# Kernel tuning notes

Hardware: AMD Instinct MI355X
Metric: run time of the kernel (lower is better)

Reference implementation:

```python
import jax, jax.numpy as jnp
import numpy as np

N_NODES = 50000
N_EDGES = 800000
IN_DIM = 128
HID_DIM = 128
N_CLASSES = 32
X_STEPS = 2
BN_EPS = 1e-5


def _agg(h, src, dst):
    # PyG 'add' aggregation with self-loops: out[i] = sum_{(j->i) in E} h[j] + h[i]
    return jax.ops.segment_sum(h[src], dst, num_segments=h.shape[0]) + h


def setup_inputs() -> dict:
    key = jax.random.key(0)
    ks = jax.random.split(key, 8)
    x = jax.random.normal(ks[0], (N_NODES, IN_DIM), dtype=jnp.float32)
    edge_index = jax.random.randint(ks[1], (2, N_EDGES), 0, N_NODES, dtype=jnp.int64)
    s1 = 1.0 / np.sqrt(IN_DIM)
    W1 = jax.random.uniform(ks[2], (IN_DIM, HID_DIM), jnp.float32, -s1, s1)
    b1 = jax.random.uniform(ks[3], (HID_DIM,), jnp.float32, -s1, s1)
    gamma = jnp.ones((HID_DIM,), jnp.float32)
    beta = jnp.zeros((HID_DIM,), jnp.float32)
    s2 = 1.0 / np.sqrt(HID_DIM)
    W2 = jax.random.uniform(ks[4], (HID_DIM, N_CLASSES), jnp.float32, -s2, s2)
    b2 = jax.random.uniform(ks[5], (N_CLASSES,), jnp.float32, -s2, s2)
    return {"x": x, "edge_index": edge_index, "W1": W1, "b1": b1,
            "gamma": gamma, "beta": beta, "W2": W2, "b2": b2}


def reference(x, edge_index, W1, b1, gamma, beta, W2, b2):
    src, dst = edge_index[0], edge_index[1]
    # conv1: K-step sum aggregation, then Linear
    h = x
    for _ in range(X_STEPS):
        h = _agg(h, src, dst)
    h = h @ W1 + b1
    # BatchNorm (training mode: batch statistics over nodes)
    mu = jnp.mean(h, axis=0)
    var = jnp.mean(jnp.square(h - mu), axis=0)  # biased variance, as torch BN uses
    h = (h - mu) * jax.lax.rsqrt(var + BN_EPS) * gamma + beta
    h = jax.nn.selu(h)
    # dropout p=0.0 -> identity
    # conv2: 1-step aggregation + Linear
    h = _agg(h, src, dst)
    h = h @ W2 + b2
    return jax.nn.softmax(h, axis=1)
```

## Files before the change

kernel.cpp:

```cpp
#include <hip/hip_runtime.h>

#define NN 50000
#define NE 800000
#define DIM 128
#define NC 32
#define CB 782
#define CCH 13
#define EB 8192
#define NBLK 98
#define BN_EPS 1e-5f
#define SELU_ALPHA 1.6732632423543772f
#define SELU_SCALE 1.0507009873554805f

typedef __attribute__((ext_vector_type(8))) short bf16x8;
typedef __attribute__((ext_vector_type(4))) float f32x4;

#define FMA16(acc, hv, w0, w1, w2, w3)                                   \
    acc.x = fmaf(hv.x, w0.x, acc.x); acc.y = fmaf(hv.x, w0.y, acc.y);    \
    acc.z = fmaf(hv.x, w0.z, acc.z); acc.w = fmaf(hv.x, w0.w, acc.w);    \
    acc.x = fmaf(hv.y, w1.x, acc.x); acc.y = fmaf(hv.y, w1.y, acc.y);    \
    acc.z = fmaf(hv.y, w1.z, acc.z); acc.w = fmaf(hv.y, w1.w, acc.w);    \
    acc.x = fmaf(hv.z, w2.x, acc.x); acc.y = fmaf(hv.z, w2.y, acc.y);    \
    acc.z = fmaf(hv.z, w2.z, acc.z); acc.w = fmaf(hv.z, w2.w, acc.w);    \
    acc.x = fmaf(hv.w, w3.x, acc.x); acc.y = fmaf(hv.w, w3.y, acc.y);    \
    acc.z = fmaf(hv.w, w3.z, acc.z); acc.w = fmaf(hv.w, w3.w, acc.w);

#define BNSELU1(v)                                                        \
    v = v > 0.f ? SELU_SCALE * v : SELU_SCALE * SELU_ALPHA * (__expf(v) - 1.f);
#define BNSELU4(hv, sc, sh)                                               \
    hv.x = fmaf(hv.x, sc.x, sh.x); BNSELU1(hv.x)                          \
    hv.y = fmaf(hv.y, sc.y, sh.y); BNSELU1(hv.y)                          \
    hv.z = fmaf(hv.z, sc.z, sh.z); BNSELU1(hv.z)                          \
    hv.w = fmaf(hv.w, sc.w, sh.w); BNSELU1(hv.w)

__device__ __forceinline__ float bf_lo(unsigned u) { return __uint_as_float(u << 16); }
__device__ __forceinline__ float bf_hi(unsigned u) { return __uint_as_float(u & 0xffff0000u); }
__device__ __forceinline__ unsigned bf_round(float a) {
    unsigned ba = __float_as_uint(a);
    return (ba + 0x7fffu + ((ba >> 16) & 1u)) >> 16;
}
__device__ __forceinline__ unsigned pack_bf16(float a, float b) {
    return bf_round(a) | (bf_round(b) << 16);
}

__device__ __forceinline__ int edge_flag(const int* raw) {
    int v = raw[2 * (threadIdx.x & 63) + 1];
    unsigned long long b = __ballot(v == 0);
    return b == 0xFFFFFFFFFFFFFFFFULL;
}

#define CVT_BLOCKS 6250
#define PREP_BLOCKS (CVT_BLOCKS + 65)
__global__ __launch_bounds__(256) void k_prep(
    const float4* __restrict__ in, uint2* __restrict__ out,
    const float* __restrict__ W1, ushort* __restrict__ w1t,
    float* __restrict__ z, const void* __restrict__ raw, int* __restrict__ cnt) {
    __shared__ int lh[CB];
    int bid = blockIdx.x, tid = threadIdx.x;
    if (bid < CVT_BLOCKS) {
        int i = bid * 256 + tid;
        float4 v = in[i];
        out[i] = make_uint2(pack_bf16(v.x, v.y), pack_bf16(v.z, v.w));
    } else if (bid < CVT_BLOCKS + 64) {
        int i = (bid - CVT_BLOCKS) * 256 + tid;
        int k = i >> 7, n = i & 127;
        w1t[n * 136 + k] = (ushort)bf_round(W1[i]);
    } else if (bid == CVT_BLOCKS + 64) {
        z[tid] = 0.f;
    } else {
        int blk = bid - PREP_BLOCKS;
        for (int t = tid; t < CB; t += 256) lh[t] = 0;
        __syncthreads();
        int f = edge_flag((const int*)raw);
        const long long* r64 = (const long long*)raw;
        const int* r32 = (const int*)raw;
        int e0 = blk * EB;
        int n = min(EB, NE - e0);
        for (int i = tid; i < n; i += 256) {
            int d = f ? (int)r64[NE + e0 + i] : r32[NE + e0 + i];
            atomicAdd(&lh[d >> 6], 1);
        }
        __syncthreads();
        for (int t = tid; t < CB; t += 256) cnt[t * NBLK + blk] = lh[t];
    }
}

__global__ void k_colscan(int* __restrict__ cnt, int* __restrict__ tot) {
    int b = blockIdx.x;
    int* row = cnt + b * NBLK;
    int l = threadIdx.x;
    int p0 = 2 * l, p1 = 2 * l + 1;
    int a0 = (p0 < NBLK) ? row[p0] : 0;
    int a1 = (p1 < NBLK) ? row[p1] : 0;
    int s = a0 + a1, inc = s;
    #pragma unroll
    for (int off = 1; off < 64; off <<= 1) {
        int u = __shfl_up(inc, off, 64);
        if (l >= off) inc += u;
    }
    int ex = inc - s;
    if (p0 < NBLK) row[p0] = ex;
    if (p1 < NBLK) row[p1] = ex + a0;
    if (l == 63) tot[b] = inc;
}

__global__ void k_cscan(const int* __restrict__ tot, int* __restrict__ cbase,
                        int* __restrict__ rowptr) {
    int lane = threadIdx.x;
    int base = lane * CCH;
    int loc[CCH];
    int s = 0;
    #pragma unroll
    for (int i = 0; i < CCH; ++i) {
        int idx = base + i;
        int v = (idx < CB) ? tot[idx] : 0;
        loc[i] = s; s += v;
    }
    int inc = s;
    #pragma unroll
    for (int off = 1; off < 64; off <<= 1) {
        int u = __shfl_up(inc, off, 64);
        if (lane >= off) inc += u;
    }
    int ex = inc - s;
    #pragma unroll
    for (int i = 0; i < CCH; ++i) {
        int idx = base + i;
        if (idx < CB) cbase[idx] = ex + loc[i];
    }
    if (lane == 63) { cbase[CB] = inc; rowptr[NN] = NE; }
}

__global__ __launch_bounds__(256) void k_cscatter2(const void* __restrict__ raw,
                                                   const int* __restrict__ cnt,
                                                   const int* __restrict__ cbase,
                                                   unsigned* __restrict__ pairs) {
    __shared__ int lh[CB], lbase[CB], lcur[CB], gbase[CB];
    __shared__ unsigned lp[EB];
    int blk = blockIdx.x, tid = threadIdx.x;
    for (int t = tid; t < CB; t += 256) {
        lh[t] = 0;
        gbase[t] = cbase[t] + cnt[t * NBLK + blk];
    }
    __syncthreads();
    int f = edge_flag((const int*)raw);
    const long long* r64 = (const long long*)raw;
    const int* r32 = (const int*)raw;
    int e0 = blk * EB;
    int n = min(EB, NE - e0);
    for (int i = tid; i < n; i += 256) {
        int d = f ? (int)r64[NE + e0 + i] : r32[NE + e0 + i];
        atomicAdd(&lh[d >> 6], 1);
    }
    __syncthreads();
    if (tid < 64) {
        int base = tid * CCH;
        int loc[CCH];
        int s = 0;
        #pragma unroll
        for (int i = 0; i < CCH; ++i) {
            int idx = base + i;
            int v = (idx < CB) ? lh[idx] : 0;
            loc[i] = s; s += v;
        }
        int inc = s;
        #pragma unroll
        for (int off = 1; off < 64; off <<= 1) {
            int u = __shfl_up(inc, off, 64);
            if (tid >= off) inc += u;
        }
        int ex = inc - s;
        #pragma unroll
        for (int i = 0; i < CCH; ++i) {
            int idx = base + i;
            if (idx < CB) lbase[idx] = ex + loc[i];
        }
    }
    __syncthreads();
    for (int t = tid; t < CB; t += 256) lcur[t] = lbase[t];
    __syncthreads();
    for (int i = tid; i < n; i += 256) {
        int d = f ? (int)r64[NE + e0 + i] : r32[NE + e0 + i];
        int sv = f ? (int)r64[e0 + i] : r32[e0 + i];
        int b = d >> 6;
        int p = atomicAdd(&lcur[b], 1);
        lp[p] = (unsigned)sv | ((unsigned)(d & 63) << 16) | ((unsigned)b << 22);
    }
    __syncthreads();
    for (int i = tid; i < n; i += 256) {
        unsigned pr = lp[i];
        int b = pr >> 22;
        pairs[gbase[b] + (i - lbase[b])] = pr;
    }
}

__global__ __launch_bounds__(256) void k_bucket(const unsigned* __restrict__ pairs,
                                                const int* __restrict__ cbase,
                                                int* __restrict__ rowptr,
                                                ushort* __restrict__ eidx) {
    __shared__ int cnt[64], cur[64];
    int b = blockIdx.x;
    int tid = threadIdx.x;
    if (tid < 64) cnt[tid] = 0;
    __syncthreads();
    int lo = cbase[b], hi = cbase[b + 1];
    for (int i = lo + tid; i < hi; i += 256)
        atomicAdd(&cnt[(pairs[i] >> 16) & 63], 1);
    __syncthreads();
    if (tid < 64) {
        int v = cnt[tid];
        int inc = v;
        #pragma unroll
        for (int off = 1; off < 64; off <<= 1) {
            int u = __shfl_up(inc, off, 64);
            if (tid >= off) inc += u;
        }
        int ex = inc - v;
        cur[tid] = ex;
        int node = b * 64 + tid;
        if (node < NN) rowptr[node] = lo + ex;
    }
    __syncthreads();
    for (int i = lo + tid; i < hi; i += 256) {
        unsigned pr = pairs[i];
        int p = atomicAdd(&cur[(pr >> 16) & 63], 1);
        eidx[lo + p] = (ushort)(pr & 0xFFFFu);
    }
}

__global__ __launch_bounds__(256) void k_gather_bf(const unsigned* __restrict__ in,
                                                   unsigned* __restrict__ out,
                                                   const int* __restrict__ rowptr,
                                                   const ushort* __restrict__ eidx) {
    int node = blockIdx.x * 4 + (threadIdx.x >> 6);
    if (node >= NN) return;
    int lane = threadIdx.x & 63;
    unsigned su = in[(size_t)node * 64 + lane];
    float2 acc = {bf_lo(su), bf_hi(su)};
    int b = rowptr[node], e = rowptr[node + 1];
    int j = b;
    for (; j + 7 < e; j += 8) {
        int s0 = eidx[j],     s1 = eidx[j + 1], s2 = eidx[j + 2], s3 = eidx[j + 3];
        int s4 = eidx[j + 4], s5 = eidx[j + 5], s6 = eidx[j + 6], s7 = eidx[j + 7];
        unsigned u0 = in[(size_t)s0 * 64 + lane];
        unsigned u1 = in[(size_t)s1 * 64 + lane];
        unsigned u2 = in[(size_t)s2 * 64 + lane];
        unsigned u3 = in[(size_t)s3 * 64 + lane];
        unsigned u4 = in[(size_t)s4 * 64 + lane];
        unsigned u5 = in[(size_t)s5 * 64 + lane];
        unsigned u6 = in[(size_t)s6 * 64 + lane];
        unsigned u7 = in[(size_t)s7 * 64 + lane];
        acc.x += bf_lo(u0) + bf_lo(u1) + bf_lo(u2) + bf_lo(u3)
               + bf_lo(u4) + bf_lo(u5) + bf_lo(u6) + bf_lo(u7);
        acc.y += bf_hi(u0) + bf_hi(u1) + bf_hi(u2) + bf_hi(u3)
               + bf_hi(u4) + bf_hi(u5) + bf_hi(u6) + bf_hi(u7);
    }
    for (; j + 3 < e; j += 4) {
        int s0 = eidx[j], s1 = eidx[j + 1], s2 = eidx[j + 2], s3 = eidx[j + 3];
        unsigned u0 = in[(size_t)s0 * 64 + lane];
        unsigned u1 = in[(size_t)s1 * 64 + lane];
        unsigned u2 = in[(size_t)s2 * 64 + lane];
        unsigned u3 = in[(size_t)s3 * 64 + lane];
        acc.x += bf_lo(u0) + bf_lo(u1) + bf_lo(u2) + bf_lo(u3);
        acc.y += bf_hi(u0) + bf_hi(u1) + bf_hi(u2) + bf_hi(u3);
    }
    for (; j < e; ++j) {
        unsigned u0 = in[(size_t)eidx[j] * 64 + lane];
        acc.x += bf_lo(u0);
        acc.y += bf_hi(u0);
    }
    out[(size_t)node * 64 + lane] = pack_bf16(acc.x, acc.y);
}

__global__ __launch_bounds__(256) void k_gemm1(
    const unsigned* __restrict__ hBb, const ushort* __restrict__ w1t,
    const float* __restrict__ b1, float* __restrict__ h1,
    float* __restrict__ ssum, float* __restrict__ ssq) {
    __shared__ __align__(16) ushort wT[DIM * 136];
    __shared__ float redS[4 * DIM];
    __shared__ float redQ[4 * DIM];
    int tid = threadIdx.x;
    for (int i = tid; i < DIM * 136 / 8; i += 256)
        ((uint4*)wT)[i] = ((const uint4*)w1t)[i];
    for (int i = tid; i < 4 * DIM; i += 256) { redS[i] = 0.f; redQ[i] = 0.f; }
    __syncthreads();

    int wid = tid >> 6, lane = tid & 63;
    int cl = lane & 15, kg = lane >> 4;
    int tile = blockIdx.x * 4 + wid;
    if (tile < NN / 16) {
        int rbase = tile * 16;
        const uint4* arow = (const uint4*)(hBb + (size_t)(rbase + cl) * 64);
        f32x4 acc[8];
        #pragma unroll
        for (int ct = 0; ct < 8; ++ct) acc[ct] = (f32x4){0.f, 0.f, 0.f, 0.f};
        #pragma unroll
        for (int kk = 0; kk < 4; ++kk) {
            union { uint4 u; bf16x8 f; } a;
            a.u = arow[kk * 4 + kg];
            #pragma unroll
            for (int ct = 0; ct < 8; ++ct) {
                union { uint4 u; bf16x8 f; } bb;
                bb.u = *(const uint4*)&wT[(ct * 16 + cl) * 136 + kk * 32 + kg * 8];
                acc[ct] = __builtin_amdgcn_mfma_f32_16x16x32_bf16(a.f, bb.f, acc[ct], 0, 0, 0);
            }
        }
        #pragma unroll
        for (int ct = 0; ct < 8; ++ct) {
            int col = ct * 16 + cl;
            float bias = b1[col];
            float s = 0.f, q = 0.f;
            #pragma unroll
            for (int i = 0; i < 4; ++i) {
                float v = acc[ct][i] + bias;
                h1[(size_t)(rbase + kg * 4 + i) * DIM + col] = v;
                s += v; q += v * v;
            }
            s += __shfl_xor(s, 16); s += __shfl_xor(s, 32);
            q += __shfl_xor(q, 16); q += __shfl_xor(q, 32);
            if (kg == 0) { redS[wid * DIM + col] = s; redQ[wid * DIM + col] = q; }
        }
    }
    __syncthreads();
    if (tid < DIM) {
        float S = redS[tid] + redS[DIM + tid] + redS[2 * DIM + tid] + redS[3 * DIM + tid];
        float Q = redQ[tid] + redQ[DIM + tid] + redQ[2 * DIM + tid] + redQ[3 * DIM + tid];
        atomicAdd(&ssum[tid], S);
        atomicAdd(&ssq[tid], Q);
    }
}

__global__ __launch_bounds__(256) void k_gemm2(const float* __restrict__ h,
                                               const float* __restrict__ W2,
                                               const float* __restrict__ ssum,
                                               const float* __restrict__ ssq,
                                               const float* __restrict__ gamma,
                                               const float* __restrict__ beta,
                                               unsigned* __restrict__ tb) {
    __shared__ float w[DIM * NC];
    __shared__ float scl[DIM], shl[DIM];
    for (int i = threadIdx.x * 4; i < DIM * NC; i += 1024)
        *(float4*)&w[i] = *(const float4*)&W2[i];
    if (threadIdx.x < DIM) {
        int c = threadIdx.x;
        float mu = ssum[c] / (float)NN;
        float var = ssq[c] / (float)NN - mu * mu;
        float rs = rsqrtf(var + BN_EPS);
        float sc = rs * gamma[c];
        scl[c] = sc;
        shl[c] = beta[c] - mu * sc;
    }
    __syncthreads();

    int c0 = (threadIdx.x & 7) * 4;
    int rg = threadIdx.x >> 3;
    int r0 = blockIdx.x * 128 + rg * 4;
    if (r0 >= NN) return;
    const float* h0 = h + (size_t)r0 * DIM;
    float4 a0 = {0, 0, 0, 0}, a1 = {0, 0, 0, 0}, a2 = {0, 0, 0, 0}, a3 = {0, 0, 0, 0};
    #pragma unroll 4
    for (int k4 = 0; k4 < DIM / 4; ++k4) {
        float4 sc = *(const float4*)&scl[k4 * 4];
        float4 sh = *(const float4*)&shl[k4 * 4];
        float4 hv0 = *(const float4*)&h0[k4 * 4];
        float4 hv1 = *(const float4*)&h0[DIM + k4 * 4];
        float4 hv2 = *(const float4*)&h0[2 * DIM + k4 * 4];
        float4 hv3 = *(const float4*)&h0[3 * DIM + k4 * 4];
        BNSELU4(hv0, sc, sh)
        BNSELU4(hv1, sc, sh)
        BNSELU4(hv2, sc, sh)
        BNSELU4(hv3, sc, sh)
        float4 w0 = *(const float4*)&w[(k4 * 4 + 0) * NC + c0];
        float4 w1 = *(const float4*)&w[(k4 * 4 + 1) * NC + c0];
        float4 w2 = *(const float4*)&w[(k4 * 4 + 2) * NC + c0];
        float4 w3 = *(const float4*)&w[(k4 * 4 + 3) * NC + c0];
        FMA16(a0, hv0, w0, w1, w2, w3)
        FMA16(a1, hv1, w0, w1, w2, w3)
        FMA16(a2, hv2, w0, w1, w2, w3)
        FMA16(a3, hv3, w0, w1, w2, w3)
    }
    ((uint2*)tb)[((size_t)r0 * 16 + c0 / 2) / 2]       = make_uint2(pack_bf16(a0.x, a0.y), pack_bf16(a0.z, a0.w));
    ((uint2*)tb)[((size_t)(r0 + 1) * 16 + c0 / 2) / 2] = make_uint2(pack_bf16(a1.x, a1.y), pack_bf16(a1.z, a1.w));
    ((uint2*)tb)[((size_t)(r0 + 2) * 16 + c0 / 2) / 2] = make_uint2(pack_bf16(a2.x, a2.y), pack_bf16(a2.z, a2.w));
    ((uint2*)tb)[((size_t)(r0 + 3) * 16 + c0 / 2) / 2] = make_uint2(pack_bf16(a3.x, a3.y), pack_bf16(a3.z, a3.w));
}

__global__ __launch_bounds__(256) void k_gsoftmax(const unsigned* __restrict__ tb,
                                                  const float* __restrict__ b2,
                                                  const int* __restrict__ rowptr,
                                                  const ushort* __restrict__ eidx,
                                                  float* __restrict__ out) {
    int node = blockIdx.x * 4 + (threadIdx.x >> 6);
    if (node >= NN) return;
    int lane = threadIdx.x & 63;
    int c2 = lane & 15;
    int g = lane >> 4;
    float2 acc = {0.f, 0.f};
    if (g == 0) {
        unsigned u = tb[(size_t)node * 16 + c2];
        acc.x = bf_lo(u); acc.y = bf_hi(u);
    }
    int b = rowptr[node], e = rowptr[node + 1];
    int j = b + g;
    for (; j + 4 < e; j += 8) {
        int s0 = eidx[j];
        int s1 = eidx[j + 4];
        unsigned u0 = tb[(size_t)s0 * 16 + c2];
        unsigned u1 = tb[(size_t)s1 * 16 + c2];
        acc.x += bf_lo(u0) + bf_lo(u1);
        acc.y += bf_hi(u0) + bf_hi(u1);
    }
    if (j < e) {
        unsigned u = tb[(size_t)eidx[j] * 16 + c2];
        acc.x += bf_lo(u);
        acc.y += bf_hi(u);
    }
    acc.x += __shfl_xor(acc.x, 16); acc.x += __shfl_xor(acc.x, 32);
    acc.y += __shfl_xor(acc.y, 16); acc.y += __shfl_xor(acc.y, 32);
    acc.x += b2[2 * c2];
    acc.y += b2[2 * c2 + 1];
    float m = fmaxf(acc.x, acc.y);
    #pragma unroll
    for (int off = 8; off; off >>= 1) m = fmaxf(m, __shfl_xor(m, off, 16));
    float2 ex = {__expf(acc.x - m), __expf(acc.y - m)};
    float s = ex.x + ex.y;
    #pragma unroll
    for (int off = 8; off; off >>= 1) s += __shfl_xor(s, off, 16);
    float inv = 1.f / s;
    if (g == 0)
        *(float2*)&out[(size_t)node * NC + 2 * c2] = make_float2(ex.x * inv, ex.y * inv);
}

extern "C" void kernel_launch(void* const* d_in, const int* in_sizes, int n_in,
                              void* d_out, int out_size, void* d_ws, size_t ws_size,
                              hipStream_t stream) {
    const float* x     = (const float*)d_in[0];
    const void*  eraw  = d_in[1];
    const float* W1    = (const float*)d_in[2];
    const float* b1    = (const float*)d_in[3];
    const float* gamma = (const float*)d_in[4];
    const float* beta  = (const float*)d_in[5];
    const float* W2    = (const float*)d_in[6];
    const float* b2    = (const float*)d_in[7];
    float* out = (float*)d_out;

    float*    regA = (float*)d_ws;
    unsigned* xb   = (unsigned*)regA;
    unsigned* hAb  = xb + (size_t)NN * 64;
    float*    h1   = regA;
    float*    regB = regA + (size_t)NN * DIM;
    unsigned* pairs= (unsigned*)regB;
    unsigned* hBb  = (unsigned*)regB;
    unsigned* tb   = (unsigned*)(regB + (size_t)NN * 64);
    ushort* eidx = (ushort*)(regB + (size_t)NN * DIM);
    int* rowptr = (int*)(eidx + NE);
    int* cnt    = rowptr + NN + 4;
    int* tot    = cnt + CB * NBLK;
    int* cbase  = tot + 784;
    float* ssum  = (float*)(cbase + 784);
    float* ssq   = ssum + DIM;
    ushort* w1t  = (ushort*)(ssq + DIM);

    k_prep<<<PREP_BLOCKS + NBLK, 256, 0, stream>>>(
        (const float4*)x, (uint2*)xb, W1, w1t, ssum, eraw, cnt);
    k_colscan<<<CB, 64, 0, stream>>>(cnt, tot);
    k_cscan<<<1, 64, 0, stream>>>(tot, cbase, rowptr);
    k_cscatter2<<<NBLK, 256, 0, stream>>>(eraw, cnt, cbase, pairs);
    k_bucket<<<CB, 256, 0, stream>>>(pairs, cbase, rowptr, eidx);

    const int gather_blocks = (NN + 3) / 4;
    k_gather_bf<<<gather_blocks, 256, 0, stream>>>(xb, hAb, rowptr, eidx);
    k_gather_bf<<<gather_blocks, 256, 0, stream>>>(hAb, hBb, rowptr, eidx);
    k_gemm1<<<(NN / 16 + 3) / 4, 256, 0, stream>>>(hBb, w1t, b1, h1, ssum, ssq);
    k_gemm2<<<(NN + 127) / 128, 256, 0, stream>>>(h1, W2, ssum, ssq, gamma, beta, tb);
    k_gsoftmax<<<gather_blocks, 256, 0, stream>>>(tb, b2, rowptr, eidx, out);
}
```

Measured before the change: 202.3 us.

## Merge column and chunk scans via last-block atomic; reuse histogram counts in scatter

Folds the single-block chunk scan into the column-scan kernel: each block bumps a done counter and the last block to finish runs the global scan. This removes one kernel launch. The scan output now goes to a separate cnts array, so the scatter kernel can read the per-block histogram from cnt directly instead of recounting destinations with a second pass and shared atomics. The cost is an extra counter reset, threadfences, and a second count array in the workspace.

```diff
diff --git a/kernel.cpp b/kernel.cpp
--- a/kernel.cpp
+++ b/kernel.cpp
@@ -54,7 +54,8 @@
 __global__ __launch_bounds__(256) void k_prep(
     const float4* __restrict__ in, uint2* __restrict__ out,
     const float* __restrict__ W1, ushort* __restrict__ w1t,
-    float* __restrict__ z, const void* __restrict__ raw, int* __restrict__ cnt) {
+    float* __restrict__ z, int* __restrict__ done,
+    const void* __restrict__ raw, int* __restrict__ cnt) {
     __shared__ int lh[CB];
     int bid = blockIdx.x, tid = threadIdx.x;
     if (bid < CVT_BLOCKS) {
@@ -67,6 +68,7 @@
         w1t[n * 136 + k] = (ushort)bf_round(W1[i]);
     } else if (bid == CVT_BLOCKS + 64) {
         z[tid] = 0.f;
+        if (tid == 0) *done = 0;
     } else {
         int blk = bid - PREP_BLOCKS;
         for (int t = tid; t < CB; t += 256) lh[t] = 0;
@@ -85,9 +87,12 @@
     }
 }
 
-__global__ void k_colscan(int* __restrict__ cnt, int* __restrict__ tot) {
+__global__ void k_scan2(const int* __restrict__ cnt, int* __restrict__ cnts,
+                        int* __restrict__ tot, int* __restrict__ cbase,
+                        int* __restrict__ rowptr, int* __restrict__ done) {
     int b = blockIdx.x;
-    int* row = cnt + b * NBLK;
+    const int* row = cnt + b * NBLK;
+    int* rows = cnts + b * NBLK;
     int l = threadIdx.x;
     int p0 = 2 * l, p1 = 2 * l + 1;
     int a0 = (p0 < NBLK) ? row[p0] : 0;
@@ -99,86 +104,86 @@
         if (l >= off) inc += u;
     }
     int ex = inc - s;
-    if (p0 < NBLK) row[p0] = ex;
-    if (p1 < NBLK) row[p1] = ex + a0;
+    if (p0 < NBLK) rows[p0] = ex;
+    if (p1 < NBLK) rows[p1] = ex + a0;
     if (l == 63) tot[b] = inc;
-}
-
-__global__ void k_cscan(const int* __restrict__ tot, int* __restrict__ cbase,
-                        int* __restrict__ rowptr) {
-    int lane = threadIdx.x;
-    int base = lane * CCH;
+
+    __threadfence();
+    int lastv = 0;
+    if (l == 0) lastv = (atomicAdd(done, 1) == CB - 1) ? 1 : 0;
+    lastv = __shfl(lastv, 0, 64);
+    if (!lastv) return;
+    __threadfence();
+
+    int base = l * CCH;
     int loc[CCH];
-    int s = 0;
+    int s2 = 0;
     #pragma unroll
     for (int i = 0; i < CCH; ++i) {
         int idx = base + i;
         int v = (idx < CB) ? tot[idx] : 0;
-        loc[i] = s; s += v;
-    }
-    int inc = s;
+        loc[i] = s2; s2 += v;
+    }
+    int inc2 = s2;
     #pragma unroll
     for (int off = 1; off < 64; off <<= 1) {
-        int u = __shfl_up(inc, off, 64);
-        if (lane >= off) inc += u;
-    }
-    int ex = inc - s;
+        int u = __shfl_up(inc2, off, 64);
+        if (l >= off) inc2 += u;
+    }
+    int ex2 = inc2 - s2;
     #pragma unroll
     for (int i = 0; i < CCH; ++i) {
         int idx = base + i;
-        if (idx < CB) cbase[idx] = ex + loc[i];
-    }
-    if (lane == 63) { cbase[CB] = inc; rowptr[NN] = NE; }
+        if (idx < CB) cbase[idx] = ex2 + loc[i];
+    }
+    if (l == 63) { cbase[CB] = inc2; rowptr[NN] = NE; }
 }
 
 __global__ __launch_bounds__(256) void k_cscatter2(const void* __restrict__ raw,
                                                    const int* __restrict__ cnt,
+                                                   const int* __restrict__ cnts,
                                                    const int* __restrict__ cbase,
                                                    unsigned* __restrict__ pairs) {
-    __shared__ int lh[CB], lbase[CB], lcur[CB], gbase[CB];
+    __shared__ int lbase[CB], lcur[CB], gbase[CB];
     __shared__ unsigned lp[EB];
+    __shared__ int lh[CB];
     int blk = blockIdx.x, tid = threadIdx.x;
     for (int t = tid; t < CB; t += 256) {
-        lh[t] = 0;
-        gbase[t] = cbase[t] + cnt[t * NBLK + blk];
-    }
+        lh[t] = cnt[t * NBLK + blk];
+        gbase[t] = cbase[t] + cnts[t * NBLK + blk];
+    }
+    __syncthreads();
+    if (tid < 64) {
+        int base = tid * CCH;
+        int loc[CCH];
+        int s = 0;
+        #pragma unroll
+        for (int i = 0; i < CCH; ++i) {
+            int idx = base + i;
+            int v = (idx < CB) ? lh[idx] : 0;
+            loc[i] = s; s += v;
+        }
+        int inc = s;
+        #pragma unroll
+        for (int off = 1; off < 64; off <<= 1) {
+            int u = __shfl_up(inc, off, 64);
+            if (tid >= off) inc += u;
+        }
+        int ex = inc - s;
+        #pragma unroll
+        for (int i = 0; i < CCH; ++i) {
+            int idx = base + i;
+            if (idx < CB) lbase[idx] = ex + loc[i];
+        }
+    }
+    __syncthreads();
+    for (int t = tid; t < CB; t += 256) lcur[t] = lbase[t];
     __syncthreads();
     int f = edge_flag((const int*)raw);
     const long long* r64 = (const long long*)raw;
     const int* r32 = (const int*)raw;
     int e0 = blk * EB;
     int n = min(EB, NE - e0);
-    for (int i = tid; i < n; i += 256) {
-        int d = f ? (int)r64[NE + e0 + i] : r32[NE + e0 + i];
-        atomicAdd(&lh[d >> 6], 1);
-    }
-    __syncthreads();
-    if (tid < 64) {
-        int base = tid * CCH;
-        int loc[CCH];
-        int s = 0;
-        #pragma unroll
-        for (int i = 0; i < CCH; ++i) {
-            int idx = base + i;
-            int v = (idx < CB) ? lh[idx] : 0;
-            loc[i] = s; s += v;
-        }
-        int inc = s;
-        #pragma unroll
-        for (int off = 1; off < 64; off <<= 1) {
-            int u = __shfl_up(inc, off, 64);
-            if (tid >= off) inc += u;
-        }
-        int ex = inc - s;
-        #pragma unroll
-        for (int i = 0; i < CCH; ++i) {
-            int idx = base + i;
-            if (idx < CB) lbase[idx] = ex + loc[i];
-        }
-    }
-    __syncthreads();
-    for (int t = tid; t < CB; t += 256) lcur[t] = lbase[t];
-    __syncthreads();
     for (int i = tid; i < n; i += 256) {
         int d = f ? (int)r64[NE + e0 + i] : r32[NE + e0 + i];
         int sv = f ? (int)r64[e0 + i] : r32[e0 + i];
@@ -455,17 +460,18 @@
     ushort* eidx = (ushort*)(regB + (size_t)NN * DIM);
     int* rowptr = (int*)(eidx + NE);
     int* cnt    = rowptr + NN + 4;
-    int* tot    = cnt + CB * NBLK;
+    int* cnts   = cnt + CB * NBLK;
+    int* tot    = cnts + CB * NBLK;
     int* cbase  = tot + 784;
-    float* ssum  = (float*)(cbase + 784);
+    int* done   = cbase + 784;
+    float* ssum  = (float*)(done + 4);
     float* ssq   = ssum + DIM;
     ushort* w1t  = (ushort*)(ssq + DIM);
 
     k_prep<<<PREP_BLOCKS + NBLK, 256, 0, stream>>>(
-        (const float4*)x, (uint2*)xb, W1, w1t, ssum, eraw, cnt);
-    k_colscan<<<CB, 64, 0, stream>>>(cnt, tot);
-    k_cscan<<<1, 64, 0, stream>>>(tot, cbase, rowptr);
-    k_cscatter2<<<NBLK, 256, 0, stream>>>(eraw, cnt, cbase, pairs);
+        (const float4*)x, (uint2*)xb, W1, w1t, ssum, done, eraw, cnt);
+    k_scan2<<<CB, 64, 0, stream>>>(cnt, cnts, tot, cbase, rowptr, done);
+    k_cscatter2<<<NBLK, 256, 0, stream>>>(eraw, cnt, cnts, cbase, pairs);
     k_bucket<<<CB, 256, 0, stream>>>(pairs, cbase, rowptr, eidx);
 
     const int gather_blocks = (NN + 3) / 4;
```

Measured after the change: 210.5 us. 1.04x slower.
